# Optimization experiments

Measured on AMD Instinct MI355X. Metric: run time of the kernel, lower is better.

## Reference

```python
import jax, jax.numpy as jnp
import numpy as np

B, S, D, F, E = 2, 1024, 1024, 4096, 8

def setup_inputs() -> dict:
    key = jax.random.key(0)
    ks = jax.random.split(key, 4)
    s = 0.02
    return {
        "x": jax.random.normal(ks[0], (B, S, D), dtype=jnp.float32),
        "switch_w": jax.random.normal(ks[1], (D, E), dtype=jnp.float32) * s,
        "switch_b": jnp.zeros((E,), dtype=jnp.float32),
        "w1": jax.random.normal(ks[2], (E, D, F), dtype=jnp.float32) * s,
        "b1": jnp.zeros((E, F), dtype=jnp.float32),
        "w2": jax.random.normal(ks[3], (E, F, D), dtype=jnp.float32) * s,
        "b2": jnp.zeros((E, D), dtype=jnp.float32),
    }

def reference(x, switch_w, switch_b, w1, b1, w2, b2):
    b, s, d = x.shape
    xt = x.reshape(-1, d)                               # [T, D]
    logits = xt @ switch_w + switch_b                   # [T, E]
    route_prob = jax.nn.softmax(logits, axis=-1)        # [T, E]
    route_prob_max = jnp.max(route_prob, axis=-1)       # [T]
    routes = jnp.argmax(route_prob, axis=-1)            # [T] int
    onehot = jax.nn.one_hot(routes, E, dtype=xt.dtype)  # [T, E]
    counts = onehot.sum(axis=0)                         # tokens per expert (float, as in torch new_tensor)

    # top-1 dispatch: run each expert FFN, keep only its tokens via mask (drop_tokens=False -> no capacity drop)
    def body(acc, params):
        W1, B1, W2, B2, mask = params                   # mask: [T]
        y = jax.nn.relu(xt @ W1 + B1) @ W2 + B2         # [T, D]
        return acc + mask[:, None] * y, None

    out, _ = jax.lax.scan(body, jnp.zeros_like(xt), (w1, b1, w2, b2, onehot.T))
    out = out * route_prob_max[:, None]                 # is_scale_prob=True
    final_output = out.reshape(b, s, d)
    return final_output, counts, route_prob.sum(axis=0), 0, route_prob_max
```

## Files before the change

kernel.cpp:

```cpp
#include <hip/hip_runtime.h>
#include <stdint.h>

#define T_TOK 2048
#define D_DIM 1024
#define F_DIM 4096
#define E_NUM 8
#define RPMAX 4096
#define BK 64

typedef __attribute__((ext_vector_type(8))) short bfx8;
typedef __attribute__((ext_vector_type(4))) float fx4;

__device__ __forceinline__ unsigned short f2bf(float f) {
  union { float f; uint32_t u; } v; v.f = f;
  uint32_t u = v.u;
  u += 0x7FFFu + ((u >> 16) & 1u);
  return (unsigned short)(u >> 16);
}

__device__ __forceinline__ void load_lds16(const unsigned short* g, unsigned short* l) {
  __builtin_amdgcn_global_load_lds(
      (const __attribute__((address_space(1))) void*)g,
      (__attribute__((address_space(3))) void*)l, 16, 0, 0);
}

__device__ __forceinline__ uint32_t cvtpk_bf16(float lo, float hi) {
  uint32_t d;
  asm("v_cvt_pk_bf16_f32 %0, %1, %2" : "=v"(d) : "v"(lo), "v"(hi));
  return d;
}

__global__ __launch_bounds__(256) void router_kernel(
    const float* __restrict__ x, const float* __restrict__ sw,
    const float* __restrict__ sb, float* __restrict__ pmax_out,
    int* __restrict__ routes, float* __restrict__ probs,
    unsigned short* __restrict__ xbf) {
  const int wave = threadIdx.x >> 6, lane = threadIdx.x & 63;
  const int t = blockIdx.x * 4 + wave;
  const float* xr = x + (size_t)t * D_DIM;
  float acc[8];
#pragma unroll
  for (int e = 0; e < 8; ++e) acc[e] = 0.f;
#pragma unroll
  for (int i = 0; i < 4; ++i) {
    const int d = i * 256 + lane * 4;
    float4 xv = *(const float4*)(xr + d);
    ushort4 h;
    h.x = f2bf(xv.x); h.y = f2bf(xv.y); h.z = f2bf(xv.z); h.w = f2bf(xv.w);
    *(ushort4*)(xbf + (size_t)t * D_DIM + d) = h;
    const float xs[4] = {xv.x, xv.y, xv.z, xv.w};
#pragma unroll
    for (int j = 0; j < 4; ++j) {
      const float4* swp = (const float4*)(sw + (size_t)(d + j) * 8);
      float4 w0 = swp[0], w1 = swp[1];
      acc[0] += xs[j] * w0.x; acc[1] += xs[j] * w0.y;
      acc[2] += xs[j] * w0.z; acc[3] += xs[j] * w0.w;
      acc[4] += xs[j] * w1.x; acc[5] += xs[j] * w1.y;
      acc[6] += xs[j] * w1.z; acc[7] += xs[j] * w1.w;
    }
  }
#pragma unroll
  for (int e = 0; e < 8; ++e) {
    float v = acc[e];
    for (int o = 32; o > 0; o >>= 1) v += __shfl_down(v, o, 64);
    acc[e] = v;
  }
  if (lane == 0) {
#pragma unroll
    for (int e = 0; e < 8; ++e) acc[e] += sb[e];
    int am = 0; float mx = acc[0];
#pragma unroll
    for (int e = 1; e < 8; ++e) if (acc[e] > mx) { mx = acc[e]; am = e; }
    float p[8]; float s = 0.f;
#pragma unroll
    for (int e = 0; e < 8; ++e) { p[e] = expf(acc[e] - mx); s += p[e]; }
    float inv = 1.0f / s;
    pmax_out[t] = inv;
    routes[t] = am;
#pragma unroll
    for (int e = 0; e < 8; ++e) probs[(size_t)t * 8 + e] = p[e] * inv;
  }
}

__global__ __launch_bounds__(256) void plan_kernel(
    const int* __restrict__ routes, const float* __restrict__ probs,
    int* __restrict__ off, int* __restrict__ perm_out, int* __restrict__ perm_src,
    float* __restrict__ out_counts, float* __restrict__ out_psums,
    float* __restrict__ out_zero) {
  __shared__ int cnt[8];
  __shared__ int cur[8];
  __shared__ int offs[9];
  __shared__ float red[256][8];
  const int tid = threadIdx.x;
  if (tid < 8) cnt[tid] = 0;
  for (int i = tid; i < RPMAX; i += 256) { perm_out[i] = -1; perm_src[i] = 0; }
  __syncthreads();
  float loc[8];
#pragma unroll
  for (int e = 0; e < 8; ++e) loc[e] = 0.f;
  for (int t = tid; t < T_TOK; t += 256) {
    atomicAdd(&cnt[routes[t]], 1);
    const float4* p = (const float4*)(probs + (size_t)t * 8);
    float4 a = p[0], b = p[1];
    loc[0] += a.x; loc[1] += a.y; loc[2] += a.z; loc[3] += a.w;
    loc[4] += b.x; loc[5] += b.y; loc[6] += b.z; loc[7] += b.w;
  }
#pragma unroll
  for (int e = 0; e < 8; ++e) red[tid][e] = loc[e];
  __syncthreads();
  for (int s = 128; s >= 1; s >>= 1) {
    if (tid < s) {
#pragma unroll
      for (int e = 0; e < 8; ++e) red[tid][e] += red[tid + s][e];
    }
    __syncthreads();
  }
  if (tid == 0) {
    int o = 0;
    for (int e = 0; e < 8; ++e) { offs[e] = o; o += ((cnt[e] + 255) >> 8) << 8; }
    offs[8] = o;
    *out_zero = 0.0f;
  }
  __syncthreads();
  if (tid < 9) off[tid] = offs[tid];
  if (tid < 8) {
    cur[tid] = offs[tid];
    out_counts[tid] = (float)cnt[tid];
    out_psums[tid] = red[0][tid];
  }
  __syncthreads();
  for (int t = tid; t < T_TOK; t += 256) {
    int e = routes[t];
    int pos = atomicAdd(&cur[e], 1);
    perm_out[pos] = t;
    perm_src[pos] = t;
  }
}

__global__ __launch_bounds__(256) void gather_kernel(
    const unsigned short* __restrict__ xbf, const int* __restrict__ off,
    const int* __restrict__ perm_src, unsigned short* __restrict__ xg) {
  const int wave = threadIdx.x >> 6, lane = threadIdx.x & 63;
  const int row = blockIdx.x * 4 + wave;
  if (row >= off[8]) return;
  const int tok = perm_src[row];
  const bfx8* s = (const bfx8*)(xbf + (size_t)tok * D_DIM);
  bfx8* d = (bfx8*)(xg + (size_t)row * D_DIM);
  d[lane] = s[lane];
  d[lane + 64] = s[lane + 64];
}

__global__ __launch_bounds__(256) void reduce_kernel(
    const float* __restrict__ P, const int* __restrict__ off,
    const int* __restrict__ perm_out, const float* __restrict__ b2,
    const float* __restrict__ pmax, float* __restrict__ out) {
  const int row = blockIdx.x;
  if (row >= off[8]) return;
  const int tok = perm_out[row];
  if (tok < 0) return;
  int e = 0;
#pragma unroll
  for (int i = 1; i <= 7; ++i) if (row >= off[i]) e = i;
  const int col = threadIdx.x * 4;
  const size_t base = (size_t)row * D_DIM + col;
  float4 p0 = *(const float4*)(P + base);
  float4 p1 = *(const float4*)(P + (size_t)1 * RPMAX * D_DIM + base);
  float4 p2 = *(const float4*)(P + (size_t)2 * RPMAX * D_DIM + base);
  float4 p3 = *(const float4*)(P + (size_t)3 * RPMAX * D_DIM + base);
  float4 bv = *(const float4*)(b2 + (size_t)e * D_DIM + col);
  const float pm = pmax[tok];
  float4 r;
  r.x = (p0.x + p1.x + p2.x + p3.x + bv.x) * pm;
  r.y = (p0.y + p1.y + p2.y + p3.y + bv.y) * pm;
  r.z = (p0.z + p1.z + p2.z + p3.z + bv.z) * pm;
  r.w = (p0.w + p1.w + p2.w + p3.w + bv.w) * pm;
  *(float4*)(out + (size_t)tok * D_DIM + col) = r;
}

template <int BN, int K_, int N_, int KSPLIT, bool FIRST>
__global__ __launch_bounds__(512, 2) void gemm256(
    const unsigned short* __restrict__ A,
    const float* __restrict__ W, const float* __restrict__ Bias,
    const int* __restrict__ off,
    unsigned short* __restrict__ Hout, float* __restrict__ Pout) {
  constexpr int BM = 256;
  constexpr int KS = K_ / KSPLIT;
  constexpr int NT = KS / BK;
  constexpr int FM = 8;
  constexpr int FN = BN / 64;
  constexpr int GRP = BN / 128;
  constexpr int NBX = N_ / BN;
  __shared__ __align__(16) unsigned short As[2][BM * 64];
  __shared__ __align__(16) unsigned short Bs[2][BN * 64];
  const int tid = threadIdx.x;
  const int nby = gridDim.y;
  const int lin = (blockIdx.z * nby + blockIdx.y) * NBX + blockIdx.x;
  const int total = NBX * nby * KSPLIT;
  const int newlin = (lin & 7) * (total >> 3) + (lin >> 3);
  const int bx = newlin / (nby * KSPLIT);
  const int rem = newlin % (nby * KSPLIT);
  const int by = rem % nby;
  const int kz = rem / nby;
  const int rowbase = by * BM;
  if (rowbase >= off[8]) return;
  int e = 0;
#pragma unroll
  for (int i = 1; i <= 7; ++i) if (rowbase >= off[i]) e = i;
  const int n0 = bx * BN;
  const int k0base = kz * KS;
  const int wave = tid >> 6, lane = tid & 63;
  const int wm = wave >> 2, wn = wave & 3;
  const float* Wn0 = W + (size_t)e * K_ * N_ + n0;

  const unsigned short* aSrc[4];
#pragma unroll
  for (int c = 0; c < 4; ++c) {
    int ca = (wave * 4 + c) * 64 + lane;
    int row = ca >> 3, slot = ca & 7;
    int sc = slot ^ (row & 7);
    aSrc[c] = A + (size_t)(rowbase + row) * K_ + k0base + sc * 8;
  }

  const int nq = lane & 15;
  const int qg = lane >> 4;
  const int kq = (qg & 1) * 4;
  fx4 br[GRP][4];

  auto A_STAGE = [&](int kt, unsigned short* Asb) {
#pragma unroll
    for (int c = 0; c < 4; ++c)
      load_lds16(aSrc[c] + kt, Asb + (wave * 4 + c) * 512);
  };
  auto B_LOAD = [&](int kt) {
#pragma unroll
    for (int g = 0; g < GRP; ++g) {
      const int cb = g * 2 + (qg >> 1);
#pragma unroll
      for (int j = 0; j < 4; ++j)
        br[g][j] = *(const fx4*)(Wn0 + (size_t)(kt + wave * 8 + kq + j) * N_ +
                                 cb * 64 + nq * 4);
    }
  };
  auto B_STORE = [&](unsigned short* Bsb) {
#pragma unroll
    for (int g = 0; g < GRP; ++g) {
      const int cb = g * 2 + (qg >> 1);
#pragma unroll
      for (int i = 0; i < 4; ++i) {
        const int nl = cb * 64 + nq * 4 + i;
        const int key = ((nl >> 2) + 2 * (nl & 3)) & 7;
        uint32_t d0 = cvtpk_bf16(br[g][0][i], br[g][1][i]);
        uint32_t d1 = cvtpk_bf16(br[g][2][i], br[g][3][i]);
        *(uint2*)(Bsb + nl * 64 + (wave ^ key) * 8 + kq) = make_uint2(d0, d1);
      }
    }
  };

  fx4 acc[FM][FN];
#pragma unroll
  for (int a = 0; a < FM; ++a)
#pragma unroll
    for (int b = 0; b < FN; ++b) acc[a][b] = (fx4){0.f, 0.f, 0.f, 0.f};

  auto COMPUTE = [&](const unsigned short* Asb, const unsigned short* Bsb) {
#pragma unroll
    for (int kk = 0; kk < 2; ++kk) {
      bfx8 af[FM], bf[FN];
#pragma unroll
      for (int fm = 0; fm < FM; ++fm) {
        int r = wm * 128 + fm * 16 + (lane & 15);
        int c = (kk * 4 + (lane >> 4)) ^ (r & 7);
        af[fm] = *(const bfx8*)(Asb + r * 64 + c * 8);
      }
#pragma unroll
      for (int fn = 0; fn < FN; ++fn) {
        int nn = wn * (BN / 4) + fn * 16 + (lane & 15);
        int key = ((nn >> 2) + 2 * (nn & 3)) & 7;
        int c = (kk * 4 + (lane >> 4)) ^ key;
        bf[fn] = *(const bfx8*)(Bsb + nn * 64 + c * 8);
      }
#pragma unroll
      for (int fm = 0; fm < FM; ++fm)
#pragma unroll
        for (int fn = 0; fn < FN; ++fn)
          acc[fm][fn] = __builtin_amdgcn_mfma_f32_16x16x32_bf16(
              af[fm], bf[fn], acc[fm][fn], 0, 0, 0);
    }
  };

  A_STAGE(0, As[0]);
  B_LOAD(0);
  B_STORE(Bs[0]);
  __syncthreads();

  for (int t = 0; t < NT; ++t) {
    const int c = t & 1;
    if (t + 1 < NT) {
      A_STAGE((t + 1) * BK, As[c ^ 1]);
      B_LOAD((t + 1) * BK);
    }
    COMPUTE(As[c], Bs[c]);
    if (t + 1 < NT) B_STORE(Bs[c ^ 1]);
    __syncthreads();
  }

  const int colbase = n0 + wn * (BN / 4);
  if (FIRST) {
#pragma unroll
    for (int fn = 0; fn < FN; ++fn) {
      int colg = colbase + fn * 16 + (lane & 15);
      float bv = Bias[(size_t)e * N_ + colg];
#pragma unroll
      for (int fm = 0; fm < FM; ++fm) {
        int rg = rowbase + wm * 128 + fm * 16 + ((lane >> 4) << 2);
#pragma unroll
        for (int j = 0; j < 4; ++j) {
          float v = fmaxf(acc[fm][fn][j] + bv, 0.f);
          Hout[(size_t)(rg + j) * N_ + colg] = f2bf(v);
        }
      }
    }
  } else {
    float* Pk = Pout + (size_t)kz * RPMAX * N_;
#pragma unroll
    for (int fm = 0; fm < FM; ++fm) {
      int rg = rowbase + wm * 128 + fm * 16 + ((lane >> 4) << 2);
#pragma unroll
      for (int j = 0; j < 4; ++j) {
#pragma unroll
        for (int fn = 0; fn < FN; ++fn) {
          int colg = colbase + fn * 16 + (lane & 15);
          Pk[(size_t)(rg + j) * N_ + colg] = acc[fm][fn][j];
        }
      }
    }
  }
}

template <int K_, int N_, int KSPLIT>
__global__ __launch_bounds__(512, 4) void gemm2s(
    const unsigned short* __restrict__ A,
    const float* __restrict__ W,
    const int* __restrict__ off,
    float* __restrict__ Pout) {
  constexpr int BM = 128, BN = 256;
  constexpr int KS = K_ / KSPLIT;
  constexpr int NT = KS / BK;
  constexpr int FM = 4, FN = 4, GRP = 2;
  constexpr int NBX = N_ / BN;
  __shared__ __align__(16) unsigned short As[BM * 64];
  __shared__ __align__(16) unsigned short Bs[BN * 64];
  const int tid = threadIdx.x;
  const int nby = gridDim.y;
  const int lin = (blockIdx.z * nby + blockIdx.y) * NBX + blockIdx.x;
  const int total = NBX * nby * KSPLIT;
  const int newlin = (lin & 7) * (total >> 3) + (lin >> 3);
  const int bx = newlin / (nby * KSPLIT);
  const int rem = newlin % (nby * KSPLIT);
  const int by = rem % nby;
  const int kz = rem / nby;
  const int rowbase = by * BM;
  if (rowbase >= off[8]) return;
  int e = 0;
#pragma unroll
  for (int i = 1; i <= 7; ++i) if (rowbase >= off[i]) e = i;
  const int n0 = bx * BN;
  const int k0base = kz * KS;
  const int wave = tid >> 6, lane = tid & 63;
  const int wm = wave >> 2, wn = wave & 3;
  const float* Wn0 = W + (size_t)e * K_ * N_ + n0;

  const unsigned short* aSrc[2];
#pragma unroll
  for (int c = 0; c < 2; ++c) {
    int ca = (wave * 2 + c) * 64 + lane;
    int row = ca >> 3, slot = ca & 7;
    int sc = slot ^ (row & 7);
    aSrc[c] = A + (size_t)(rowbase + row) * K_ + k0base + sc * 8;
  }

  const int nq = lane & 15;
  const int qg = lane >> 4;
  const int kq = (qg & 1) * 4;
  fx4 br[GRP][4];

  fx4 acc[FM][FN];
#pragma unroll
  for (int a = 0; a < FM; ++a)
#pragma unroll
    for (int b = 0; b < FN; ++b) acc[a][b] = (fx4){0.f, 0.f, 0.f, 0.f};

  for (int t = 0; t < NT; ++t) {
    const int kt = t * BK;
#pragma unroll
    for (int c = 0; c < 2; ++c)
      load_lds16(aSrc[c] + kt, As + (wave * 2 + c) * 512);
#pragma unroll
    for (int g = 0; g < GRP; ++g) {
      const int cb = g * 2 + (qg >> 1);
#pragma unroll
      for (int j = 0; j < 4; ++j)
        br[g][j] = *(const fx4*)(Wn0 + (size_t)(kt + wave * 8 + kq + j) * N_ +
                                 cb * 64 + nq * 4);
    }
#pragma unroll
    for (int g = 0; g < GRP; ++g) {
      const int cb = g * 2 + (qg >> 1);
#pragma unroll
      for (int i = 0; i < 4; ++i) {
        const int nl = cb * 64 + nq * 4 + i;
        const int key = ((nl >> 2) + 2 * (nl & 3)) & 7;
        uint32_t d0 = cvtpk_bf16(br[g][0][i], br[g][1][i]);
        uint32_t d1 = cvtpk_bf16(br[g][2][i], br[g][3][i]);
        *(uint2*)(Bs + nl * 64 + (wave ^ key) * 8 + kq) = make_uint2(d0, d1);
      }
    }
    __syncthreads();
#pragma unroll
    for (int kk = 0; kk < 2; ++kk) {
      bfx8 af[FM], bf[FN];
#pragma unroll
      for (int fm = 0; fm < FM; ++fm) {
        int r = wm * 64 + fm * 16 + (lane & 15);
        int c = (kk * 4 + (lane >> 4)) ^ (r & 7);
        af[fm] = *(const bfx8*)(As + r * 64 + c * 8);
      }
#pragma unroll
      for (int fn = 0; fn < FN; ++fn) {
        int nn = wn * 64 + fn * 16 + (lane & 15);
        int key = ((nn >> 2) + 2 * (nn & 3)) & 7;
        int c = (kk * 4 + (lane >> 4)) ^ key;
        bf[fn] = *(const bfx8*)(Bs + nn * 64 + c * 8);
      }
#pragma unroll
      for (int fm = 0; fm < FM; ++fm)
#pragma unroll
        for (int fn = 0; fn < FN; ++fn)
          acc[fm][fn] = __builtin_amdgcn_mfma_f32_16x16x32_bf16(
              af[fm], bf[fn], acc[fm][fn], 0, 0, 0);
    }
    __syncthreads();
  }

  const int colbase = n0 + wn * 64;
  float* Pk = Pout + (size_t)kz * RPMAX * N_;
#pragma unroll
  for (int fm = 0; fm < FM; ++fm) {
    int rg = rowbase + wm * 64 + fm * 16 + ((lane >> 4) << 2);
#pragma unroll
    for (int j = 0; j < 4; ++j) {
#pragma unroll
      for (int fn = 0; fn < FN; ++fn) {
        int colg = colbase + fn * 16 + (lane & 15);
        Pk[(size_t)(rg + j) * N_ + colg] = acc[fm][fn][j];
      }
    }
  }
}

extern "C" void kernel_launch(void* const* d_in, const int* in_sizes, int n_in,
                              void* d_out, int out_size, void* d_ws, size_t ws_size,
                              hipStream_t stream) {
  const float* x  = (const float*)d_in[0];
  const float* sw = (const float*)d_in[1];
  const float* sb = (const float*)d_in[2];
  const float* w1 = (const float*)d_in[3];
  const float* b1 = (const float*)d_in[4];
  const float* w2 = (const float*)d_in[5];
  const float* b2 = (const float*)d_in[6];
  float* out = (float*)d_out;

  char* ws = (char*)d_ws;
  int*   off      = (int*)(ws + 0);
  int*   routes   = (int*)(ws + 1024);
  int*   perm_out = (int*)(ws + 16384);
  int*   perm_src = (int*)(ws + 32768);
  float* probs    = (float*)(ws + 65536);
  unsigned short* xbf = (unsigned short*)(ws + (1u << 20));
  unsigned short* H   = (unsigned short*)(ws + (8u << 20));
  unsigned short* xg  = (unsigned short*)(ws + (40u << 20));
  float* P            = (float*)(ws + (48u << 20));

  float* out_final  = out;
  float* out_counts = out + 2097152;
  float* out_psums  = out + 2097160;
  float* out_zero   = out + 2097168;
  float* out_pmax   = out + 2097169;

  router_kernel<<<T_TOK / 4, 256, 0, stream>>>(x, sw, sb, out_pmax, routes, probs, xbf);
  plan_kernel<<<1, 256, 0, stream>>>(routes, probs, off, perm_out, perm_src,
                                     out_counts, out_psums, out_zero);
  gather_kernel<<<RPMAX / 4, 256, 0, stream>>>(xbf, off, perm_src, xg);

  gemm256<256, D_DIM, F_DIM, 1, true>
      <<<dim3(F_DIM / 256, RPMAX / 256, 1), 512, 0, stream>>>(
          xg, w1, b1, off, H, nullptr);
  gemm2s<F_DIM, D_DIM, 4>
      <<<dim3(D_DIM / 256, RPMAX / 128, 4), 512, 0, stream>>>(H, w2, off, P);
  reduce_kernel<<<RPMAX, 256, 0, stream>>>(P, off, perm_out, b2, out_pmax, out_final);
}
```

Baseline: 132.7 us.

## Replace double-buffered 256x256 first GEMM with single-buffered 128x256 tile kernel

The first expert GEMM moves from a 256-row, double-buffered tile kernel (launch bounds 2 blocks/CU) to a 128-row, single-buffered kernel with launch bounds of 4 blocks/CU, mirroring the existing gemm2s design. Smaller LDS and register footprint allows more resident blocks and twice as many row tiles, which gives finer granularity over the expert row padding. In exchange, prefetch overlap within a block is lost and each W1 tile is re-read and re-converted by twice as many row blocks.

```diff
diff --git a/kernel.cpp b/kernel.cpp
--- a/kernel.cpp
+++ b/kernel.cpp
@@ -177,48 +177,43 @@
   *(float4*)(out + (size_t)tok * D_DIM + col) = r;
 }
 
-template <int BN, int K_, int N_, int KSPLIT, bool FIRST>
-__global__ __launch_bounds__(512, 2) void gemm256(
+template <int K_, int N_>
+__global__ __launch_bounds__(512, 4) void gemm1s(
     const unsigned short* __restrict__ A,
-    const float* __restrict__ W, const float* __restrict__ Bias,
+    const float* __restrict__ W,
+    const float* __restrict__ Bias,
     const int* __restrict__ off,
-    unsigned short* __restrict__ Hout, float* __restrict__ Pout) {
-  constexpr int BM = 256;
-  constexpr int KS = K_ / KSPLIT;
-  constexpr int NT = KS / BK;
-  constexpr int FM = 8;
-  constexpr int FN = BN / 64;
-  constexpr int GRP = BN / 128;
+    unsigned short* __restrict__ Hout) {
+  constexpr int BM = 128, BN = 256;
+  constexpr int NT = K_ / BK;
+  constexpr int FM = 4, FN = 4, GRP = 2;
   constexpr int NBX = N_ / BN;
-  __shared__ __align__(16) unsigned short As[2][BM * 64];
-  __shared__ __align__(16) unsigned short Bs[2][BN * 64];
+  __shared__ __align__(16) unsigned short As[BM * 64];
+  __shared__ __align__(16) unsigned short Bs[BN * 64];
   const int tid = threadIdx.x;
   const int nby = gridDim.y;
-  const int lin = (blockIdx.z * nby + blockIdx.y) * NBX + blockIdx.x;
-  const int total = NBX * nby * KSPLIT;
+  const int lin = blockIdx.y * NBX + blockIdx.x;
+  const int total = NBX * nby;
   const int newlin = (lin & 7) * (total >> 3) + (lin >> 3);
-  const int bx = newlin / (nby * KSPLIT);
-  const int rem = newlin % (nby * KSPLIT);
-  const int by = rem % nby;
-  const int kz = rem / nby;
+  const int bx = newlin / nby;
+  const int by = newlin % nby;
   const int rowbase = by * BM;
   if (rowbase >= off[8]) return;
   int e = 0;
 #pragma unroll
   for (int i = 1; i <= 7; ++i) if (rowbase >= off[i]) e = i;
   const int n0 = bx * BN;
-  const int k0base = kz * KS;
   const int wave = tid >> 6, lane = tid & 63;
   const int wm = wave >> 2, wn = wave & 3;
   const float* Wn0 = W + (size_t)e * K_ * N_ + n0;
 
-  const unsigned short* aSrc[4];
-#pragma unroll
-  for (int c = 0; c < 4; ++c) {
-    int ca = (wave * 4 + c) * 64 + lane;
+  const unsigned short* aSrc[2];
+#pragma unroll
+  for (int c = 0; c < 2; ++c) {
+    int ca = (wave * 2 + c) * 64 + lane;
     int row = ca >> 3, slot = ca & 7;
     int sc = slot ^ (row & 7);
-    aSrc[c] = A + (size_t)(rowbase + row) * K_ + k0base + sc * 8;
+    aSrc[c] = A + (size_t)(rowbase + row) * K_ + sc * 8;
   }
 
   const int nq = lane & 15;
@@ -226,12 +221,17 @@
   const int kq = (qg & 1) * 4;
   fx4 br[GRP][4];
 
-  auto A_STAGE = [&](int kt, unsigned short* Asb) {
-#pragma unroll
-    for (int c = 0; c < 4; ++c)
-      load_lds16(aSrc[c] + kt, Asb + (wave * 4 + c) * 512);
-  };
-  auto B_LOAD = [&](int kt) {
+  fx4 acc[FM][FN];
+#pragma unroll
+  for (int a = 0; a < FM; ++a)
+#pragma unroll
+    for (int b = 0; b < FN; ++b) acc[a][b] = (fx4){0.f, 0.f, 0.f, 0.f};
+
+  for (int t = 0; t < NT; ++t) {
+    const int kt = t * BK;
+#pragma unroll
+    for (int c = 0; c < 2; ++c)
+      load_lds16(aSrc[c] + kt, As + (wave * 2 + c) * 512);
 #pragma unroll
     for (int g = 0; g < GRP; ++g) {
       const int cb = g * 2 + (qg >> 1);
@@ -240,8 +240,6 @@
         br[g][j] = *(const fx4*)(Wn0 + (size_t)(kt + wave * 8 + kq + j) * N_ +
                                  cb * 64 + nq * 4);
     }
-  };
-  auto B_STORE = [&](unsigned short* Bsb) {
 #pragma unroll
     for (int g = 0; g < GRP; ++g) {
       const int cb = g * 2 + (qg >> 1);
@@ -251,33 +249,25 @@
         const int key = ((nl >> 2) + 2 * (nl & 3)) & 7;
         uint32_t d0 = cvtpk_bf16(br[g][0][i], br[g][1][i]);
         uint32_t d1 = cvtpk_bf16(br[g][2][i], br[g][3][i]);
-        *(uint2*)(Bsb + nl * 64 + (wave ^ key) * 8 + kq) = make_uint2(d0, d1);
-      }
-    }
-  };
-
-  fx4 acc[FM][FN];
-#pragma unroll
-  for (int a = 0; a < FM; ++a)
-#pragma unroll
-    for (int b = 0; b < FN; ++b) acc[a][b] = (fx4){0.f, 0.f, 0.f, 0.f};
-
-  auto COMPUTE = [&](const unsigned short* Asb, const unsigned short* Bsb) {
+        *(uint2*)(Bs + nl * 64 + (wave ^ key) * 8 + kq) = make_uint2(d0, d1);
+      }
+    }
+    __syncthreads();
 #pragma unroll
     for (int kk = 0; kk < 2; ++kk) {
       bfx8 af[FM], bf[FN];
 #pragma unroll
       for (int fm = 0; fm < FM; ++fm) {
-        int r = wm * 128 + fm * 16 + (lane & 15);
+        int r = wm * 64 + fm * 16 + (lane & 15);
         int c = (kk * 4 + (lane >> 4)) ^ (r & 7);
-        af[fm] = *(const bfx8*)(Asb + r * 64 + c * 8);
+        af[fm] = *(const bfx8*)(As + r * 64 + c * 8);
       }
 #pragma unroll
       for (int fn = 0; fn < FN; ++fn) {
-        int nn = wn * (BN / 4) + fn * 16 + (lane & 15);
+        int nn = wn * 64 + fn * 16 + (lane & 15);
         int key = ((nn >> 2) + 2 * (nn & 3)) & 7;
         int c = (kk * 4 + (lane >> 4)) ^ key;
-        bf[fn] = *(const bfx8*)(Bsb + nn * 64 + c * 8);
+        bf[fn] = *(const bfx8*)(Bs + nn * 64 + c * 8);
       }
 #pragma unroll
       for (int fm = 0; fm < FM; ++fm)
@@ -286,52 +276,21 @@
           acc[fm][fn] = __builtin_amdgcn_mfma_f32_16x16x32_bf16(
               af[fm], bf[fn], acc[fm][fn], 0, 0, 0);
     }
-  };
-
-  A_STAGE(0, As[0]);
-  B_LOAD(0);
-  B_STORE(Bs[0]);
-  __syncthreads();
-
-  for (int t = 0; t < NT; ++t) {
-    const int c = t & 1;
-    if (t + 1 < NT) {
-      A_STAGE((t + 1) * BK, As[c ^ 1]);
-      B_LOAD((t + 1) * BK);
-    }
-    COMPUTE(As[c], Bs[c]);
-    if (t + 1 < NT) B_STORE(Bs[c ^ 1]);
     __syncthreads();
   }
 
-  const int colbase = n0 + wn * (BN / 4);
-  if (FIRST) {
-#pragma unroll
-    for (int fn = 0; fn < FN; ++fn) {
-      int colg = colbase + fn * 16 + (lane & 15);
-      float bv = Bias[(size_t)e * N_ + colg];
-#pragma unroll
-      for (int fm = 0; fm < FM; ++fm) {
-        int rg = rowbase + wm * 128 + fm * 16 + ((lane >> 4) << 2);
-#pragma unroll
-        for (int j = 0; j < 4; ++j) {
-          float v = fmaxf(acc[fm][fn][j] + bv, 0.f);
-          Hout[(size_t)(rg + j) * N_ + colg] = f2bf(v);
-        }
-      }
-    }
-  } else {
-    float* Pk = Pout + (size_t)kz * RPMAX * N_;
+  const int colbase = n0 + wn * 64;
+#pragma unroll
+  for (int fn = 0; fn < FN; ++fn) {
+    int colg = colbase + fn * 16 + (lane & 15);
+    float bv = Bias[(size_t)e * N_ + colg];
 #pragma unroll
     for (int fm = 0; fm < FM; ++fm) {
-      int rg = rowbase + wm * 128 + fm * 16 + ((lane >> 4) << 2);
+      int rg = rowbase + wm * 64 + fm * 16 + ((lane >> 4) << 2);
 #pragma unroll
       for (int j = 0; j < 4; ++j) {
-#pragma unroll
-        for (int fn = 0; fn < FN; ++fn) {
-          int colg = colbase + fn * 16 + (lane & 15);
-          Pk[(size_t)(rg + j) * N_ + colg] = acc[fm][fn][j];
-        }
+        float v = fmaxf(acc[fm][fn][j] + bv, 0.f);
+        Hout[(size_t)(rg + j) * N_ + colg] = f2bf(v);
       }
     }
   }
@@ -492,9 +451,9 @@
                                      out_counts, out_psums, out_zero);
   gather_kernel<<<RPMAX / 4, 256, 0, stream>>>(xbf, off, perm_src, xg);
 
-  gemm256<256, D_DIM, F_DIM, 1, true>
-      <<<dim3(F_DIM / 256, RPMAX / 256, 1), 512, 0, stream>>>(
-          xg, w1, b1, off, H, nullptr);
+  gemm1s<D_DIM, F_DIM>
+      <<<dim3(F_DIM / 256, RPMAX / 128, 1), 512, 0, stream>>>(
+          xg, w1, b1, off, H);
   gemm2s<F_DIM, D_DIM, 4>
       <<<dim3(D_DIM / 256, RPMAX / 128, 4), 512, 0, stream>>>(H, w2, off, P);
   reduce_kernel<<<RPMAX, 256, 0, stream>>>(P, off, perm_out, b2, out_pmax, out_final);
```

New measurement: 131.3 us, median of 3. About the same (-1.0%).
